# Optimization experiments

Measured on AMD Instinct MI355X. Metric: run time of the kernel, lower is better.

## Reference

```python
import jax, jax.numpy as jnp
import numpy as np

B, L, D_MODEL = 2, 1024, 1024
EXPAND = 2
D_INNER = EXPAND * D_MODEL      # 2048
D_STATE = 16
D_CONV = 4
DT_RANK = D_MODEL // 16         # 64


def setup_inputs() -> dict:
    key = jax.random.key(0)
    ks = jax.random.split(key, 8)
    s = 0.02
    x = jax.random.normal(ks[0], (B, L, D_MODEL), jnp.float32)
    W_in = (jax.random.normal(ks[1], (D_MODEL, 2 * D_INNER), jnp.float32) * s)
    conv_w = jax.random.normal(ks[2], (D_INNER, 1, D_CONV), jnp.float32) * 0.2  # depthwise kernel (O,I/g,K)
    conv_b = jnp.zeros((D_INNER,), jnp.float32)
    W_xproj = jax.random.normal(ks[3], (D_INNER, DT_RANK + 2 * D_STATE), jnp.float32) * s
    W_dt = jax.random.normal(ks[4], (DT_RANK, D_INNER), jnp.float32) * (DT_RANK ** -0.5)
    b_dt = jnp.full((D_INNER,), -4.6, jnp.float32)  # softplus^{-1}(~0.01), mamba-style dt init
    A_log = jnp.log(jnp.broadcast_to(jnp.arange(1, D_STATE + 1, dtype=jnp.float32), (D_INNER, D_STATE)))
    D_skip = jnp.ones((D_INNER,), jnp.float32)
    W_out = jax.random.normal(ks[5], (D_INNER, D_MODEL), jnp.float32) * s
    return dict(x=x, W_in=W_in, conv_w=conv_w, conv_b=conv_b, W_xproj=W_xproj,
                W_dt=W_dt, b_dt=b_dt, A_log=A_log, D_skip=D_skip, W_out=W_out)


def _mamba(x, W_in, conv_w, conv_b, W_xproj, W_dt, b_dt, A_log, D_skip, W_out):
    b, l, _ = x.shape
    # input projection and gate split
    xz = jnp.einsum('bld,de->ble', x, W_in)            # (B, L, 2*d_inner)
    x_in, z = jnp.split(xz, 2, axis=-1)                # each (B, L, d_inner)
    # causal depthwise conv1d + SiLU
    xt = jnp.transpose(x_in, (0, 2, 1))                # (B, d_inner, L)
    xt = jnp.pad(xt, ((0, 0), (0, 0), (D_CONV - 1, 0)))
    conv = jax.lax.conv_general_dilated(
        xt, conv_w, window_strides=(1,), padding='VALID',
        dimension_numbers=('NCH', 'OIH', 'NCH'), feature_group_count=D_INNER)
    conv = conv + conv_b[None, :, None]                # (B, d_inner, L)
    u = jax.nn.silu(jnp.transpose(conv, (0, 2, 1)))    # (B, L, d_inner)
    # input-dependent SSM parameters
    x_dbl = jnp.einsum('bld,de->ble', u, W_xproj)      # (B, L, dt_rank + 2*d_state)
    dt_lr = x_dbl[..., :DT_RANK]
    Bm = x_dbl[..., DT_RANK:DT_RANK + D_STATE]         # (B, L, d_state)
    Cm = x_dbl[..., DT_RANK + D_STATE:]                # (B, L, d_state)
    delta = jax.nn.softplus(jnp.einsum('blr,rd->bld', dt_lr, W_dt) + b_dt)  # (B, L, d_inner)
    A = -jnp.exp(A_log)                                # (d_inner, d_state)
    dA = jnp.exp(jnp.einsum('bld,dn->bldn', delta, A))           # (B, L, d_inner, d_state)
    dBu = (delta * u)[..., None] * Bm[:, :, None, :]              # (B, L, d_inner, d_state)
    # selective scan over time
    def step(h, inp):
        dA_t, dBu_t, C_t = inp
        h = dA_t * h + dBu_t                           # (B, d_inner, d_state)
        y_t = jnp.einsum('bdn,bn->bd', h, C_t)
        return h, y_t
    h0 = jnp.zeros((b, D_INNER, D_STATE), x.dtype)
    _, ys = jax.lax.scan(step, h0, (jnp.swapaxes(dA, 0, 1), jnp.swapaxes(dBu, 0, 1), jnp.swapaxes(Cm, 0, 1)))
    y = jnp.swapaxes(ys, 0, 1)                          # (B, L, d_inner)
    y = y + D_skip * u
    y = y * jax.nn.silu(z)
    out = jnp.einsum('bld,de->ble', y, W_out)           # (B, L, d_model)
    return out  # dropout is identity in eval mode


def reference(x, W_in, conv_w, conv_b, W_xproj, W_dt, b_dt, A_log, D_skip, W_out):
    return _mamba(x, W_in, conv_w, conv_b, W_xproj, W_dt, b_dt, A_log, D_skip, W_out)
```

## Files before the change

### kernel.cpp

```cpp
#include <hip/hip_runtime.h>
#include <cmath>

#define B_  2
#define L_  1024
#define DM  1024
#define DI  2048
#define DS  16
#define DR  64
#define NC  32
#define CL  (L_/NC)

typedef __attribute__((ext_vector_type(8))) short short8;
typedef __attribute__((ext_vector_type(4))) float f32x4;

static __device__ __forceinline__ ushort f2bf(float f) {
    union { float f; unsigned u; } c; c.f = f;
    unsigned u = c.u;
    return (ushort)((u + 0x7fffu + ((u >> 16) & 1u)) >> 16);
}
static __device__ __forceinline__ float bf2f(ushort h) {
    union { unsigned u; float f; } c; c.u = ((unsigned)h) << 16;
    return c.f;
}

static __device__ __forceinline__ float softplus_f(float v) {
    return (v > 20.f) ? v : log1pf(__expf(v));
}

static __device__ void bt_body(const float* __restrict__ in,
                               ushort* __restrict__ oh, ushort* __restrict__ ol,
                               int K, int N, int Npad, int bx, int by,
                               float (*t)[33])
{
    const int tid = threadIdx.x;
    const int tx = tid & 31, ty = tid >> 5;
    const int n0 = bx * 32, k0 = by * 32;
    #pragma unroll
    for (int i = 0; i < 4; ++i) {
        int k = k0 + ty * 4 + i, n = n0 + tx;
        t[ty * 4 + i][tx] = (n < N) ? in[(size_t)k * N + n] : 0.f;
    }
    __syncthreads();
    #pragma unroll
    for (int i = 0; i < 4; ++i) {
        int r = n0 + ty * 4 + i;
        int c = k0 + tx;
        if (r < Npad) {
            float v = t[tx][ty * 4 + i];
            ushort h = f2bf(v);
            oh[(size_t)r * K + c] = h;
            if (ol) ol[(size_t)r * K + c] = f2bf(v - bf2f(h));
        }
    }
}

__global__ __launch_bounds__(256) void prep_all(
    const float* __restrict__ x, const float* __restrict__ W_in,
    const float* __restrict__ W_xprj, const float* __restrict__ W_dt,
    ushort* __restrict__ Xh, ushort* __restrict__ WIh,
    ushort* __restrict__ WXh, ushort* __restrict__ WXl,
    ushort* __restrict__ WDh, ushort* __restrict__ WDl)
{
    __shared__ float t[32][33];
    int blk = blockIdx.x;
    if (blk < 4096) {
        bt_body(W_in, WIh, nullptr, 1024, 4096, 4096, blk & 127, blk >> 7, t);
    } else if (blk < 4352) {
        int b2 = blk - 4096;
        bt_body(W_xprj, WXh, WXl, 2048, 96, 128, b2 & 3, b2 >> 2, t);
    } else if (blk < 4480) {
        int b2 = blk - 4352;
        bt_body(W_dt, WDh, WDl, 64, 2048, 2048, b2 & 63, b2 >> 6, t);
    } else {
        int v = (blk - 4480) * 256 + threadIdx.x;
        int r  = v >> 7;
        int c8 = v & 127;
        const float* p = x + (size_t)r * DM + c8 * 8;
        float4 v0 = *(const float4*)p;
        float4 v1 = *(const float4*)(p + 4);
        float vv[8] = {v0.x, v0.y, v0.z, v0.w, v1.x, v1.y, v1.z, v1.w};
        unsigned h[4];
        #pragma unroll
        for (int j = 0; j < 4; ++j)
            h[j] = (unsigned)f2bf(vv[2*j]) | ((unsigned)f2bf(vv[2*j+1]) << 16);
        size_t o = (size_t)r * 1024 + c8 * 8;
        *(uint4*)&Xh[o] = make_uint4(h[0], h[1], h[2], h[3]);
    }
}

__global__ __launch_bounds__(256) void convBT(
    const float* __restrict__ in, ushort* __restrict__ oh,
    int K, int N, int Npad)
{
    __shared__ float t[32][33];
    bt_body(in, oh, nullptr, K, N, Npad, blockIdx.x, blockIdx.y, t);
}

static __device__ __forceinline__ void stage_tile(
    ushort* lds, const ushort* __restrict__ g, int ld, int row0, int k0,
    int wid, int lane)
{
    #pragma unroll
    for (int it = 0; it < 2; ++it) {
        int o  = wid * 2048 + it * 1024;
        int ob = o + lane * 16;
        int a  = ob ^ (((ob >> 7) & 7) << 4);
        int row = a >> 6;
        int lc  = (a >> 4) & 3;
        const ushort* gp = g + (size_t)(row0 + row) * ld + k0 + lc * 8;
        __builtin_amdgcn_global_load_lds(
            (const __attribute__((address_space(1))) void*)gp,
            (__attribute__((address_space(3))) void*)((char*)lds + o),
            16, 0, 0);
    }
}

static __device__ __forceinline__ void stage_tile64(
    ushort* lds, const ushort* __restrict__ g, int ld, int row0, int k0,
    int wid, int lane)
{
    int o  = wid * 1024;
    int ob = o + lane * 16;
    int a  = ob ^ (((ob >> 7) & 7) << 4);
    int row = a >> 6;
    int lc  = (a >> 4) & 3;
    const ushort* gp = g + (size_t)(row0 + row) * ld + k0 + lc * 8;
    __builtin_amdgcn_global_load_lds(
        (const __attribute__((address_space(1))) void*)gp,
        (__attribute__((address_space(3))) void*)((char*)lds + o),
        16, 0, 0);
}

static __device__ __forceinline__ short8 frag(const ushort* lds, int row, int fq) {
    int a = row * 64 + fq * 16;
    int b = a ^ (((a >> 7) & 7) << 4);
    return *(const short8*)((const char*)lds + b);
}

template<int TERMS>
static __device__ __forceinline__ void stage_all(
    ushort* buf, const ushort* Ah, const ushort* Bh, const ushort* Bl,
    int lda, int ldb, int bm, int bn, int k, int wid, int lane)
{
    stage_tile(buf,        Ah, lda, bm, k, wid, lane);
    stage_tile(buf + 4096, Bh, ldb, bn, k, wid, lane);
    if (TERMS == 2) stage_tile(buf + 8192, Bl, ldb, bn, k, wid, lane);
}

template<int TERMS>
static __device__ __forceinline__ void compute_tile(
    const ushort* buf, int wr, int wc, int fr, int fq, f32x4 acc[4][4])
{
    const ushort* sAh = buf;
    const ushort* sBh = buf + 4096;
    const ushort* sBl = buf + 8192;
    short8 a_h[4], b_h[4], b_l[4];
    #pragma unroll
    for (int m = 0; m < 4; ++m)
        a_h[m] = frag(sAh, wr + m * 16 + fr, fq);
    #pragma unroll
    for (int n = 0; n < 4; ++n) {
        b_h[n] = frag(sBh, wc + n * 16 + fr, fq);
        if (TERMS == 2) b_l[n] = frag(sBl, wc + n * 16 + fr, fq);
    }
    #pragma unroll
    for (int m = 0; m < 4; ++m)
        #pragma unroll
        for (int n = 0; n < 4; ++n) {
            acc[m][n] = __builtin_amdgcn_mfma_f32_16x16x32_bf16(a_h[m], b_h[n], acc[m][n], 0, 0, 0);
            if (TERMS == 2)
                acc[m][n] = __builtin_amdgcn_mfma_f32_16x16x32_bf16(a_h[m], b_l[n], acc[m][n], 0, 0, 0);
        }
}

template<int TERMS, int EPI>
__global__ __launch_bounds__(256) void gemm_bt(
    const ushort* __restrict__ Ah,
    const ushort* __restrict__ Bh, const ushort* __restrict__ Bl,
    float* __restrict__ C, ushort* __restrict__ oh, ushort* __restrict__ ol,
    const float* __restrict__ bvec,
    int M, int N, int lda, int ldb, int ldc, int kspl)
{
    constexpr int TILE = TERMS == 1 ? 8192 : 12288;
    __shared__ ushort sm[2 * TILE];

    const int tid = threadIdx.x, wid = tid >> 6, lane = tid & 63;
    const int bm = blockIdx.y * 128, bn = blockIdx.x * 128;
    const int kb = blockIdx.z * kspl;
    const int wr = (wid >> 1) * 64, wc = (wid & 1) * 64;
    const int fr = lane & 15, fq = lane >> 4;

    f32x4 acc[4][4] = {};

    stage_all<TERMS>(sm, Ah, Bh, Bl, lda, ldb, bm, bn, kb, wid, lane);
    __syncthreads();
    int cur = 0;
    for (int k0 = 32; k0 < kspl; k0 += 32) {
        ushort* nbuf       = cur ? sm : sm + TILE;
        const ushort* cbuf = cur ? sm + TILE : sm;
        stage_all<TERMS>(nbuf, Ah, Bh, Bl, lda, ldb, bm, bn, kb + k0, wid, lane);
        compute_tile<TERMS>(cbuf, wr, wc, fr, fq, acc);
        __syncthreads();
        cur ^= 1;
    }
    compute_tile<TERMS>(cur ? sm + TILE : sm, wr, wc, fr, fq, acc);

    #pragma unroll
    for (int m = 0; m < 4; ++m) {
        int rbase = bm + wr + m * 16 + fq * 4;
        #pragma unroll
        for (int n = 0; n < 4; ++n) {
            int col = bn + wc + n * 16 + fr;
            if (col >= N) continue;
            if (EPI == 0) {
                #pragma unroll
                for (int j = 0; j < 4; ++j)
                    C[((size_t)blockIdx.z * M + rbase + j) * ldc + col] = acc[m][n][j];
            } else {
                float bb = bvec[col];
                #pragma unroll
                for (int j = 0; j < 4; ++j) {
                    float v = softplus_f(acc[m][n][j] + bb);
                    ushort hh = f2bf(v);
                    size_t off = (size_t)(rbase + j) * ldc + col;
                    oh[off] = hh;
                    ol[off] = f2bf(v - bf2f(hh));
                }
            }
        }
    }
}

__global__ __launch_bounds__(256) void gemm_out64(
    const ushort* __restrict__ Ah, const ushort* __restrict__ Bh,
    float* __restrict__ C, int K, int lda, int ldb, int ldc)
{
    __shared__ ushort sm[12288];
    const int tid = threadIdx.x, wid = tid >> 6, lane = tid & 63;
    const int bm = blockIdx.y * 128, bn = blockIdx.x * 64;
    const int wr = (wid >> 1) * 64, wc = (wid & 1) * 32;
    const int fr = lane & 15, fq = lane >> 4;

    f32x4 acc[4][2] = {};

    stage_tile  (sm,        Ah, lda, bm, 0, wid, lane);
    stage_tile64(sm + 4096, Bh, ldb, bn, 0, wid, lane);
    __syncthreads();
    int cur = 0;
    for (int k0 = 32; k0 < K; k0 += 32) {
        ushort* nbuf       = cur ? sm : sm + 6144;
        const ushort* cbuf = cur ? sm + 6144 : sm;
        stage_tile  (nbuf,        Ah, lda, bm, k0, wid, lane);
        stage_tile64(nbuf + 4096, Bh, ldb, bn, k0, wid, lane);
        {
            short8 a_h[4], b_h[2];
            #pragma unroll
            for (int m = 0; m < 4; ++m)
                a_h[m] = frag(cbuf, wr + m * 16 + fr, fq);
            #pragma unroll
            for (int n = 0; n < 2; ++n)
                b_h[n] = frag(cbuf + 4096, wc + n * 16 + fr, fq);
            #pragma unroll
            for (int m = 0; m < 4; ++m)
                #pragma unroll
                for (int n = 0; n < 2; ++n)
                    acc[m][n] = __builtin_amdgcn_mfma_f32_16x16x32_bf16(a_h[m], b_h[n], acc[m][n], 0, 0, 0);
        }
        __syncthreads();
        cur ^= 1;
    }
    {
        const ushort* cbuf = cur ? sm + 6144 : sm;
        short8 a_h[4], b_h[2];
        #pragma unroll
        for (int m = 0; m < 4; ++m)
            a_h[m] = frag(cbuf, wr + m * 16 + fr, fq);
        #pragma unroll
        for (int n = 0; n < 2; ++n)
            b_h[n] = frag(cbuf + 4096, wc + n * 16 + fr, fq);
        #pragma unroll
        for (int m = 0; m < 4; ++m)
            #pragma unroll
            for (int n = 0; n < 2; ++n)
                acc[m][n] = __builtin_amdgcn_mfma_f32_16x16x32_bf16(a_h[m], b_h[n], acc[m][n], 0, 0, 0);
    }

    #pragma unroll
    for (int m = 0; m < 4; ++m) {
        int rbase = bm + wr + m * 16 + fq * 4;
        #pragma unroll
        for (int n = 0; n < 2; ++n) {
            int col = bn + wc + n * 16 + fr;
            #pragma unroll
            for (int j = 0; j < 4; ++j)
                C[(size_t)(rbase + j) * ldc + col] = acc[m][n][j];
        }
    }
}

__global__ __launch_bounds__(256) void reduce_xproj(
    const float* __restrict__ p, float* __restrict__ xdbl,
    ushort* __restrict__ DTh)
{
    int i = blockIdx.x * 256 + threadIdx.x;
    if (i >= 2048 * 96) return;
    float s = 0.f;
    #pragma unroll
    for (int c = 0; c < 8; ++c) s += p[i + (size_t)c * (2048 * 96)];
    xdbl[i] = s;
    int row = i / 96, col = i - row * 96;
    if (col < 64) DTh[row * 64 + col] = f2bf(s);
}

__global__ __launch_bounds__(256) void conv_silu(
    const float* __restrict__ xz, const float* __restrict__ w,
    const float* __restrict__ bias, ushort* __restrict__ uh,
    ushort* __restrict__ ul)
{
    int idx = blockIdx.x * 256 + threadIdx.x;
    if (idx >= B_ * L_ * DI) return;
    int d  = idx & (DI - 1);
    int bl = idx >> 11;
    int l  = bl & (L_ - 1);

    const float w0 = w[d * 4 + 0], w1 = w[d * 4 + 1];
    const float w2 = w[d * 4 + 2], w3 = w[d * 4 + 3];
    float s = bias[d];
    size_t base = (size_t)bl * 4096 + d;
    if (l >= 3) s = fmaf(w0, xz[base - 3 * 4096], s);
    if (l >= 2) s = fmaf(w1, xz[base - 2 * 4096], s);
    if (l >= 1) s = fmaf(w2, xz[base - 1 * 4096], s);
    s = fmaf(w3, xz[base], s);
    float v = s / (1.f + __expf(-s));
    ushort h = f2bf(v);
    uh[idx] = h;
    ul[idx] = f2bf(v - bf2f(h));
}

__global__ __launch_bounds__(256) void scan_partial(
    const ushort* __restrict__ Dh, const ushort* __restrict__ Dl,
    const ushort* __restrict__ uh, const ushort* __restrict__ ul,
    const float* __restrict__ xdbl, const float* __restrict__ A_log,
    float* __restrict__ sA, float* __restrict__ sH)
{
    __shared__ float Bs[CL][16];
    const int tid  = threadIdx.x;
    const int dblk = blockIdx.x & 7;
    const int c    = (blockIdx.x >> 3) & (NC - 1);
    const int b    = blockIdx.x >> 8;
    const int d    = dblk * 256 + tid;
    const int bl0  = b * L_ + c * CL;

    for (int i = tid; i < CL * 16; i += 256) {
        int t = i >> 4, n = i & 15;
        Bs[t][n] = xdbl[(size_t)(bl0 + t) * 96 + DR + n];
    }
    __syncthreads();

    float Adn[16];
    #pragma unroll
    for (int q = 0; q < 4; ++q) {
        float4 al = *(const float4*)&A_log[d * DS + q * 4];
        Adn[q * 4 + 0] = -__expf(al.x);
        Adn[q * 4 + 1] = -__expf(al.y);
        Adn[q * 4 + 2] = -__expf(al.z);
        Adn[q * 4 + 3] = -__expf(al.w);
    }
    float h[16];
    #pragma unroll
    for (int n = 0; n < 16; ++n) h[n] = 0.f;
    float S = 0.f;

    size_t pd = (size_t)bl0 * DI + d;
    for (int t = 0; t < CL; ++t) {
        float dv = bf2f(Dh[pd]) + bf2f(Dl[pd]);
        float uv = bf2f(uh[pd]) + bf2f(ul[pd]);
        float du = dv * uv;
        S += dv;
        float Bv[16];
        *(float4*)&Bv[0]  = *(const float4*)&Bs[t][0];
        *(float4*)&Bv[4]  = *(const float4*)&Bs[t][4];
        *(float4*)&Bv[8]  = *(const float4*)&Bs[t][8];
        *(float4*)&Bv[12] = *(const float4*)&Bs[t][12];
        #pragma unroll
        for (int n = 0; n < 16; ++n) {
            float dA = __expf(dv * Adn[n]);
            h[n] = fmaf(dA, h[n], du * Bv[n]);
        }
        pd += DI;
    }

    size_t o = (((size_t)c * B_ + b) * DI + d) * DS;
    float aP[16], hh[16];
    #pragma unroll
    for (int n = 0; n < 16; ++n) { aP[n] = __expf(S * Adn[n]); hh[n] = h[n]; }
    #pragma unroll
    for (int q = 0; q < 4; ++q) {
        *(float4*)&sA[o + q * 4] = *(float4*)&aP[q * 4];
        *(float4*)&sH[o + q * 4] = *(float4*)&hh[q * 4];
    }
}

__global__ __launch_bounds__(256) void scan_combine(
    const float* __restrict__ sA, const float* __restrict__ sH,
    float* __restrict__ hinit)
{
    int idx = blockIdx.x * 256 + threadIdx.x;
    int n = idx & 15;
    int d = (idx >> 4) & (DI - 1);
    int b = idx >> 15;
    float h = 0.f;
    #pragma unroll
    for (int c = 0; c < NC; ++c) {
        size_t o = (((size_t)c * B_ + b) * DI + d) * DS + n;
        hinit[o] = h;
        h = fmaf(sA[o], h, sH[o]);
    }
}

__global__ __launch_bounds__(256) void scan_final(
    const ushort* __restrict__ Dh, const ushort* __restrict__ Dl,
    const ushort* __restrict__ uh, const ushort* __restrict__ ul,
    const float* __restrict__ xdbl, const float* __restrict__ xz,
    const float* __restrict__ A_log, const float* __restrict__ D_skip,
    const float* __restrict__ hinit, ushort* __restrict__ yh)
{
    __shared__ float Bs[CL][16];
    __shared__ float Cs[CL][16];
    const int tid  = threadIdx.x;
    const int dblk = blockIdx.x & 7;
    const int c    = (blockIdx.x >> 3) & (NC - 1);
    const int b    = blockIdx.x >> 8;
    const int d    = dblk * 256 + tid;
    const int bl0  = b * L_ + c * CL;

    for (int i = tid; i < CL * 16; i += 256) {
        int t = i >> 4, n = i & 15;
        size_t px = (size_t)(bl0 + t) * 96 + DR + n;
        Bs[t][n] = xdbl[px];
        Cs[t][n] = xdbl[px + DS];
    }
    __syncthreads();

    float Adn[16];
    #pragma unroll
    for (int q = 0; q < 4; ++q) {
        float4 al = *(const float4*)&A_log[d * DS + q * 4];
        Adn[q * 4 + 0] = -__expf(al.x);
        Adn[q * 4 + 1] = -__expf(al.y);
        Adn[q * 4 + 2] = -__expf(al.z);
        Adn[q * 4 + 3] = -__expf(al.w);
    }
    const float Dd = D_skip[d];

    float h[16];
    size_t o = (((size_t)c * B_ + b) * DI + d) * DS;
    #pragma unroll
    for (int q = 0; q < 4; ++q)
        *(float4*)&h[q * 4] = *(const float4*)&hinit[o + q * 4];

    size_t pd = (size_t)bl0 * DI + d;
    size_t pz = (size_t)bl0 * 4096 + 2048 + d;
    for (int t = 0; t < CL; ++t) {
        float dv = bf2f(Dh[pd]) + bf2f(Dl[pd]);
        float uv = bf2f(uh[pd]) + bf2f(ul[pd]);
        float du = dv * uv;
        float Bv[16], Cv[16];
        *(float4*)&Bv[0]  = *(const float4*)&Bs[t][0];
        *(float4*)&Bv[4]  = *(const float4*)&Bs[t][4];
        *(float4*)&Bv[8]  = *(const float4*)&Bs[t][8];
        *(float4*)&Bv[12] = *(const float4*)&Bs[t][12];
        *(float4*)&Cv[0]  = *(const float4*)&Cs[t][0];
        *(float4*)&Cv[4]  = *(const float4*)&Cs[t][4];
        *(float4*)&Cv[8]  = *(const float4*)&Cs[t][8];
        *(float4*)&Cv[12] = *(const float4*)&Cs[t][12];
        float acc = 0.f;
        #pragma unroll
        for (int n = 0; n < 16; ++n) {
            float dA = __expf(dv * Adn[n]);
            h[n] = fmaf(dA, h[n], du * Bv[n]);
            acc = fmaf(h[n], Cv[n], acc);
        }
        float zv = xz[pz];
        float yv = acc + Dd * uv;
        yv *= zv / (1.f + __expf(-zv));
        yh[pd] = f2bf(yv);
        pd += DI; pz += 4096;
    }
}

extern "C" void kernel_launch(void* const* d_in, const int* in_sizes, int n_in,
                              void* d_out, int out_size, void* d_ws, size_t ws_size,
                              hipStream_t stream)
{
    const float* x      = (const float*)d_in[0];
    const float* W_in   = (const float*)d_in[1];
    const float* conv_w = (const float*)d_in[2];
    const float* conv_b = (const float*)d_in[3];
    const float* W_xprj = (const float*)d_in[4];
    const float* W_dt   = (const float*)d_in[5];
    const float* b_dt   = (const float*)d_in[6];
    const float* A_log  = (const float*)d_in[7];
    const float* D_skip = (const float*)d_in[8];
    const float* W_out  = (const float*)d_in[9];
    float* out = (float*)d_out;

    char* ws = (char*)d_ws;
    float*  xz    = (float*)(ws + 0);
    ushort* Dh    = (ushort*)(ws + 33554432);
    ushort* Dl    = (ushort*)(ws + 41943040);
    float*  xdbl  = (float*)(ws + 50331648);
    ushort* Xh    = (ushort*)(ws + 57409536);
    float*  parts = (float*)(ws + 57409536);
    ushort* WIh   = (ushort*)(ws + 65798144);
    float*  sA    = (float*)(ws + 57409536);
    float*  sH    = (float*)(ws + 65798144);
    float*  hin   = (float*)(ws + 74186752);
    ushort* Yh    = (ushort*)(ws + 57409536);
    ushort* Uh    = (ushort*)(ws + 82575360);
    ushort* Ul    = (ushort*)(ws + 90963968);
    ushort* Woh   = (ushort*)(ws + 82575360);
    ushort* WXh   = (ushort*)(ws + 99352576);
    ushort* WXl   = (ushort*)(ws + 99876864);
    ushort* DTh   = (ushort*)(ws + 100401152);
    ushort* WDh   = (ushort*)(ws + 100914176);
    ushort* WDl   = (ushort*)(ws + 101170688);

    dim3 blk(256);
    const int M = B_ * L_;

    prep_all<<<dim3(5504), blk, 0, stream>>>(
        x, W_in, W_xprj, W_dt, Xh, WIh, WXh, WXl, WDh, WDl);

    gemm_bt<1, 0><<<dim3(32, 16, 1), blk, 0, stream>>>(
        Xh, WIh, nullptr, xz, nullptr, nullptr, nullptr,
        M, 4096, DM, DM, 4096, DM);

    conv_silu<<<dim3((B_ * L_ * DI) / 256), blk, 0, stream>>>(xz, conv_w, conv_b, Uh, Ul);

    gemm_bt<2, 0><<<dim3(1, 16, 8), blk, 0, stream>>>(
        Uh, WXh, WXl, parts, nullptr, nullptr, nullptr,
        M, 96, DI, DI, 96, 256);
    reduce_xproj<<<dim3(768), blk, 0, stream>>>(parts, xdbl, DTh);

    gemm_bt<2, 1><<<dim3(16, 16, 1), blk, 0, stream>>>(
        DTh, WDh, WDl, nullptr, Dh, Dl, b_dt,
        M, DI, DR, DR, DI, DR);

    scan_partial<<<dim3(B_ * NC * 8), blk, 0, stream>>>(
        Dh, Dl, Uh, Ul, xdbl, A_log, sA, sH);
    scan_combine<<<dim3((B_ * DI * DS) / 256), blk, 0, stream>>>(sA, sH, hin);
    scan_final<<<dim3(B_ * NC * 8), blk, 0, stream>>>(
        Dh, Dl, Uh, Ul, xdbl, xz, A_log, D_skip, hin, Yh);

    convBT<<<dim3(DM / 32, DI / 32), blk, 0, stream>>>(W_out, Woh, DI, DM, DM);
    gemm_out64<<<dim3(DM / 64, M / 128), blk, 0, stream>>>(
        Yh, Woh, out, DI, DI, DI, DM);
}
```

Before: 181.9 us.

## Drop u low-bf16 part, fold W_out transpose into prep, deeper xproj split-K

Stores the conv+SiLU output u as a single bf16 value instead of a hi/lo pair. This removes one write stream in conv_silu and one read stream in both scan kernels. It also moves the W_out transpose/convert into the prep_all launch, removing a separate kernel launch, and doubles the split-K factor of the x_proj GEMM from 8 to 16 with a matching reduction. The cost is lower precision of u in the scans and the x_proj GEMM, plus twice as many partial sums to reduce.

```diff
diff --git a/kernel.cpp b/kernel.cpp
--- a/kernel.cpp
+++ b/kernel.cpp
@@ -57,9 +57,11 @@
 __global__ __launch_bounds__(256) void prep_all(
     const float* __restrict__ x, const float* __restrict__ W_in,
     const float* __restrict__ W_xprj, const float* __restrict__ W_dt,
+    const float* __restrict__ W_out,
     ushort* __restrict__ Xh, ushort* __restrict__ WIh,
     ushort* __restrict__ WXh, ushort* __restrict__ WXl,
-    ushort* __restrict__ WDh, ushort* __restrict__ WDl)
+    ushort* __restrict__ WDh, ushort* __restrict__ WDl,
+    ushort* __restrict__ Woh)
 {
     __shared__ float t[32][33];
     int blk = blockIdx.x;
@@ -71,7 +73,7 @@
     } else if (blk < 4480) {
         int b2 = blk - 4352;
         bt_body(W_dt, WDh, WDl, 64, 2048, 2048, b2 & 63, b2 >> 6, t);
-    } else {
+    } else if (blk < 5504) {
         int v = (blk - 4480) * 256 + threadIdx.x;
         int r  = v >> 7;
         int c8 = v & 127;
@@ -85,15 +87,10 @@
             h[j] = (unsigned)f2bf(vv[2*j]) | ((unsigned)f2bf(vv[2*j+1]) << 16);
         size_t o = (size_t)r * 1024 + c8 * 8;
         *(uint4*)&Xh[o] = make_uint4(h[0], h[1], h[2], h[3]);
-    }
-}
-
-__global__ __launch_bounds__(256) void convBT(
-    const float* __restrict__ in, ushort* __restrict__ oh,
-    int K, int N, int Npad)
-{
-    __shared__ float t[32][33];
-    bt_body(in, oh, nullptr, K, N, Npad, blockIdx.x, blockIdx.y, t);
+    } else {
+        int b2 = blk - 5504;
+        bt_body(W_out, Woh, nullptr, 2048, 1024, 1024, b2 & 31, b2 >> 5, t);
+    }
 }
 
 static __device__ __forceinline__ void stage_tile(
@@ -306,7 +303,7 @@
     if (i >= 2048 * 96) return;
     float s = 0.f;
     #pragma unroll
-    for (int c = 0; c < 8; ++c) s += p[i + (size_t)c * (2048 * 96)];
+    for (int c = 0; c < 16; ++c) s += p[i + (size_t)c * (2048 * 96)];
     xdbl[i] = s;
     int row = i / 96, col = i - row * 96;
     if (col < 64) DTh[row * 64 + col] = f2bf(s);
@@ -314,8 +311,7 @@
 
 __global__ __launch_bounds__(256) void conv_silu(
     const float* __restrict__ xz, const float* __restrict__ w,
-    const float* __restrict__ bias, ushort* __restrict__ uh,
-    ushort* __restrict__ ul)
+    const float* __restrict__ bias, ushort* __restrict__ uh)
 {
     int idx = blockIdx.x * 256 + threadIdx.x;
     if (idx >= B_ * L_ * DI) return;
@@ -332,14 +328,12 @@
     if (l >= 1) s = fmaf(w2, xz[base - 1 * 4096], s);
     s = fmaf(w3, xz[base], s);
     float v = s / (1.f + __expf(-s));
-    ushort h = f2bf(v);
-    uh[idx] = h;
-    ul[idx] = f2bf(v - bf2f(h));
+    uh[idx] = f2bf(v);
 }
 
 __global__ __launch_bounds__(256) void scan_partial(
     const ushort* __restrict__ Dh, const ushort* __restrict__ Dl,
-    const ushort* __restrict__ uh, const ushort* __restrict__ ul,
+    const ushort* __restrict__ uh,
     const float* __restrict__ xdbl, const float* __restrict__ A_log,
     float* __restrict__ sA, float* __restrict__ sH)
 {
@@ -374,7 +368,7 @@
     size_t pd = (size_t)bl0 * DI + d;
     for (int t = 0; t < CL; ++t) {
         float dv = bf2f(Dh[pd]) + bf2f(Dl[pd]);
-        float uv = bf2f(uh[pd]) + bf2f(ul[pd]);
+        float uv = bf2f(uh[pd]);
         float du = dv * uv;
         S += dv;
         float Bv[16];
@@ -420,7 +414,7 @@
 
 __global__ __launch_bounds__(256) void scan_final(
     const ushort* __restrict__ Dh, const ushort* __restrict__ Dl,
-    const ushort* __restrict__ uh, const ushort* __restrict__ ul,
+    const ushort* __restrict__ uh,
     const float* __restrict__ xdbl, const float* __restrict__ xz,
     const float* __restrict__ A_log, const float* __restrict__ D_skip,
     const float* __restrict__ hinit, ushort* __restrict__ yh)
@@ -463,7 +457,7 @@
     size_t pz = (size_t)bl0 * 4096 + 2048 + d;
     for (int t = 0; t < CL; ++t) {
         float dv = bf2f(Dh[pd]) + bf2f(Dl[pd]);
-        float uv = bf2f(uh[pd]) + bf2f(ul[pd]);
+        float uv = bf2f(uh[pd]);
         float du = dv * uv;
         float Bv[16], Cv[16];
         *(float4*)&Bv[0]  = *(const float4*)&Bs[t][0];
@@ -510,6 +504,7 @@
     ushort* Dh    = (ushort*)(ws + 33554432);
     ushort* Dl    = (ushort*)(ws + 41943040);
     float*  xdbl  = (float*)(ws + 50331648);
+    ushort* Woh   = (ushort*)(ws + 51118080);
     ushort* Xh    = (ushort*)(ws + 57409536);
     float*  parts = (float*)(ws + 57409536);
     ushort* WIh   = (ushort*)(ws + 65798144);
@@ -518,8 +513,6 @@
     float*  hin   = (float*)(ws + 74186752);
     ushort* Yh    = (ushort*)(ws + 57409536);
     ushort* Uh    = (ushort*)(ws + 82575360);
-    ushort* Ul    = (ushort*)(ws + 90963968);
-    ushort* Woh   = (ushort*)(ws + 82575360);
     ushort* WXh   = (ushort*)(ws + 99352576);
     ushort* WXl   = (ushort*)(ws + 99876864);
     ushort* DTh   = (ushort*)(ws + 100401152);
@@ -529,18 +522,18 @@
     dim3 blk(256);
     const int M = B_ * L_;
 
-    prep_all<<<dim3(5504), blk, 0, stream>>>(
-        x, W_in, W_xprj, W_dt, Xh, WIh, WXh, WXl, WDh, WDl);
+    prep_all<<<dim3(7552), blk, 0, stream>>>(
+        x, W_in, W_xprj, W_dt, W_out, Xh, WIh, WXh, WXl, WDh, WDl, Woh);
 
     gemm_bt<1, 0><<<dim3(32, 16, 1), blk, 0, stream>>>(
         Xh, WIh, nullptr, xz, nullptr, nullptr, nullptr,
         M, 4096, DM, DM, 4096, DM);
 
-    conv_silu<<<dim3((B_ * L_ * DI) / 256), blk, 0, stream>>>(xz, conv_w, conv_b, Uh, Ul);
-
-    gemm_bt<2, 0><<<dim3(1, 16, 8), blk, 0, stream>>>(
+    conv_silu<<<dim3((B_ * L_ * DI) / 256), blk, 0, stream>>>(xz, conv_w, conv_b, Uh);
+
+    gemm_bt<2, 0><<<dim3(1, 16, 16), blk, 0, stream>>>(
         Uh, WXh, WXl, parts, nullptr, nullptr, nullptr,
-        M, 96, DI, DI, 96, 256);
+        M, 96, DI, DI, 96, 128);
     reduce_xproj<<<dim3(768), blk, 0, stream>>>(parts, xdbl, DTh);
 
     gemm_bt<2, 1><<<dim3(16, 16, 1), blk, 0, stream>>>(
@@ -548,12 +541,11 @@
         M, DI, DR, DR, DI, DR);
 
     scan_partial<<<dim3(B_ * NC * 8), blk, 0, stream>>>(
-        Dh, Dl, Uh, Ul, xdbl, A_log, sA, sH);
+        Dh, Dl, Uh, xdbl, A_log, sA, sH);
     scan_combine<<<dim3((B_ * DI * DS) / 256), blk, 0, stream>>>(sA, sH, hin);
     scan_final<<<dim3(B_ * NC * 8), blk, 0, stream>>>(
-        Dh, Dl, Uh, Ul, xdbl, xz, A_log, D_skip, hin, Yh);
-
-    convBT<<<dim3(DM / 32, DI / 32), blk, 0, stream>>>(W_out, Woh, DI, DM, DM);
+        Dh, Dl, Uh, xdbl, xz, A_log, D_skip, hin, Yh);
+
     gemm_out64<<<dim3(DM / 64, M / 128), blk, 0, stream>>>(
         Yh, Woh, out, DI, DI, DI, DM);
 }
```

New measurement: 175.4 us. 1.04x faster.
